# Kernel tuning notes

Hardware: AMD Instinct MI355X
Metric: run time of the kernel (lower is better)

The kernel has to match this reference:

```python
import jax, jax.numpy as jnp
import numpy as np
import math

NFREQ = 257
NFILTERS = 64
IN_DIM = 64
HIDDEN = 128
SR = 16000
B = 2
T = 1000


def _mel_bounds():
    # Exact replica of FreqCompression.__init__ bound computation (htk mel scale).
    all_freqs = np.linspace(0.0, SR // 2, NFREQ)
    m_max = 2595.0 * math.log10(1.0 + (SR / 2.0) / 700.0)
    m_pts = np.linspace(0.0, m_max, NFILTERS + 2)
    f_pts = 700.0 * (10.0 ** (m_pts / 2595.0) - 1.0)
    bounds = [0]
    for i in range(1, NFILTERS + 1):
        bounds.append(int(np.argmax(all_freqs > f_pts[i])))
    bounds.append(NFREQ)
    return bounds


def setup_inputs() -> dict:
    key = jax.random.key(0)
    k1, k2 = jax.random.split(key)
    bounds = _mel_bounds()
    widths = np.array([bounds[f + 2] - bounds[f] for f in range(NFILTERS)])
    jmax = int(widths.max())
    starts = np.array(bounds[:NFILTERS])
    # per-band freq-bin gather indices, clamped padding
    idx = np.clip(starts[:, None] + np.arange(jmax)[None, :], 0, NFREQ - 1)
    mask = (np.arange(jmax)[None, :] < widths[:, None]).astype(np.float32)  # (F, Jmax)
    x = jax.random.normal(k1, (B, IN_DIM, T, NFREQ), dtype=jnp.float32)
    # Padded ragged trans1 weights: band f uses a (HIDDEN, width_f*IN_DIM) Linear (no bias).
    # Zero-masked beyond each band's true width so padded gather lanes contribute nothing.
    W = jax.random.normal(k2, (NFILTERS, HIDDEN, IN_DIM, jmax), dtype=jnp.float32) * 0.05
    W = W * jnp.asarray(mask)[:, None, None, :]
    return {"x": x, "W": W, "idx": jnp.asarray(idx, jnp.int32), "inverse": 0}


def reference(x, W, idx, inverse):
    # Forward (compression) branch of FreqCompression.forward (inverse == 0).
    # Original: x -> (B, T, in_dim, F); per band f: flatten x[..., bounds[f]:bounds[f+2]]
    # over (in_dim, width) and apply bias-free Linear -> (B, T, hidden); stack over bands
    # and permute to (B, hidden, T, nfilters). Expressed as one padded gather + einsum:
    # x: (B, C, T, F_full); idx: (F, J); W: (F, H, C, J) zero-masked past band width.
    xg = x[:, :, :, idx]  # (B, C, T, F, J)
    out = jnp.einsum('bctfj,fhcj->bhtf', xg, W)  # (B, H, T, F)
    return out
```

## Files before the change

### kernel.cpp

```cpp
#include <hip/hip_runtime.h>
#include <hip/hip_bf16.h>

#define B_    2
#define C_    64
#define T_    1000
#define NF_   257
#define F_    64
#define H_    128
#define NFP_  288

typedef __bf16  bfv8  __attribute__((ext_vector_type(8)));
typedef float   f32x4 __attribute__((ext_vector_type(4)));
typedef short   s16x8 __attribute__((ext_vector_type(8)));

#define GLOBAL_AS __attribute__((address_space(1)))
#define SHARED_AS __attribute__((address_space(3)))

static __device__ __forceinline__ short f2bf(float f) {
  __hip_bfloat16 h = __float2bfloat16(f);
  return *reinterpret_cast<short*>(&h);
}

static __device__ __forceinline__ void gload_lds16(const void* g, void* l) {
  __builtin_amdgcn_global_load_lds((const GLOBAL_AS void*)g, (SHARED_AS void*)l, 16, 0, 0);
}

__global__ __launch_bounds__(256) void xprep_kernel(const float* __restrict__ x,
                                                    short* __restrict__ xT) {
  __shared__ float Ls[64][33];
  const int k0 = blockIdx.x * 32;
  const int t  = blockIdx.y;
  const int b  = blockIdx.z;
  {
    const int k  = threadIdx.x & 31;
    const int cb = threadIdx.x >> 5;
#pragma unroll
    for (int i = 0; i < 8; ++i) {
      int c = cb + 8 * i;
      float f = 0.0f;
      int kk = k0 + k;
      if (kk < NF_) f = x[(((size_t)(b * C_ + c)) * T_ + t) * NF_ + kk];
      Ls[c][k] = f;
    }
  }
  __syncthreads();
  {
    const int k  = threadIdx.x >> 3;
    const int c0 = (threadIdx.x & 7) * 8;
    s16x8 v;
#pragma unroll
    for (int i = 0; i < 8; ++i) v[i] = f2bf(Ls[c0 + i][k]);
    *reinterpret_cast<s16x8*>(&xT[(((size_t)(b * T_ + t)) * NFP_ + k0 + k) * C_ + c0]) = v;
  }
}

__global__ __launch_bounds__(256) void wprep_kernel(const float* __restrict__ W,
                                                    short* __restrict__ Wp,
                                                    int* __restrict__ wwidth,
                                                    int jmax, int JPAD) {
  extern __shared__ short Lw[];
  __shared__ int smax;
  const int f  = blockIdx.x >> 4;
  const int h8 = (blockIdx.x & 15) * 8;
  const int tid = threadIdx.x;
  if (tid == 0) smax = 0;
  __syncthreads();
  const int chunk = 8 * C_ * jmax;
  const float* src = W + ((size_t)(f * H_ + h8)) * C_ * jmax;
  int lm = -1;
  for (int o = tid; o < chunk; o += 256) {
    float v = src[o];
    Lw[o] = f2bf(v);
    if (v != 0.0f) { int j = o % jmax; if (j > lm) lm = j; }
  }
  atomicMax(&smax, lm + 1);
  __syncthreads();
  if (tid == 0) atomicMax(&wwidth[f], smax);
  const int KP = C_ * JPAD;
  const int nv = 8 * JPAD * 8;
  for (int id = tid; id < nv; id += 256) {
    int c0 = (id & 7) * 8;
    int j  = (id >> 3) % JPAD;
    int h  = (id >> 3) / JPAD;
    s16x8 v;
    if (j < jmax) {
#pragma unroll
      for (int u = 0; u < 8; ++u) v[u] = Lw[h * C_ * jmax + (c0 + u) * jmax + j];
    } else {
      short z = f2bf(0.0f);
#pragma unroll
      for (int u = 0; u < 8; ++u) v[u] = z;
    }
    *reinterpret_cast<s16x8*>(&Wp[((size_t)(f * H_ + h8 + h)) * KP + j * C_ + c0]) = v;
  }
}

__global__ __launch_bounds__(256) void gemm_kernel(const short* __restrict__ xT,
                                                   const short* __restrict__ Wp,
                                                   const int* __restrict__ idx,
                                                   const int* __restrict__ wwidth,
                                                   float* __restrict__ tmp,
                                                   int jmax, int JPAD) {
  __shared__ short As[128 * 64];
  __shared__ short Ws[128 * 64];
  const int id = blockIdx.x;
  const int sw = (id & 7) * 128 + (id >> 3);
  const int f  = sw & 63;
  const int tb = sw >> 6;
  const int tt = tb & 7;
  const int b  = tb >> 3;
  const int t0 = tt * 128;
  const int tid  = threadIdx.x;
  const int wave = tid >> 6;
  const int lane = tid & 63;
  const int wm = wave >> 1, wn = wave & 1;
  const int start = idx[f * jmax];
  const int KP = C_ * JPAD;
  int wf = wwidth[f];
  if (wf > JPAD) wf = JPAD;

  f32x4 acc[4][4] = {};

  const int srow = wave * 32 + (lane >> 3);
  const int scol = (lane & 7) * 8;

  for (int j = 0; j < wf; ++j) {
    __syncthreads();
#pragma unroll
    for (int i = 0; i < 4; ++i) {
      int r = srow + i * 8;
      int tc = t0 + r; if (tc >= T_) tc = T_ - 1;
      const short* src = &xT[(((size_t)(b * T_ + tc)) * NFP_ + (start + j)) * C_ + scol];
      gload_lds16(src, &As[(wave * 32 + i * 8) * 64]);
    }
#pragma unroll
    for (int i = 0; i < 4; ++i) {
      int h = srow + i * 8;
      const short* src = &Wp[((size_t)(f * H_ + h)) * KP + j * 64 + scol];
      gload_lds16(src, &Ws[(wave * 32 + i * 8) * 64]);
    }
    __syncthreads();
#pragma unroll
    for (int ks = 0; ks < 2; ++ks) {
      bfv8 a[4], w[4];
#pragma unroll
      for (int mi = 0; mi < 4; ++mi)
        a[mi] = *reinterpret_cast<const bfv8*>(
            &As[(wm * 64 + mi * 16 + (lane & 15)) * 64 + ks * 32 + (lane >> 4) * 8]);
#pragma unroll
      for (int ni = 0; ni < 4; ++ni)
        w[ni] = *reinterpret_cast<const bfv8*>(
            &Ws[(wn * 64 + ni * 16 + (lane & 15)) * 64 + ks * 32 + (lane >> 4) * 8]);
#pragma unroll
      for (int mi = 0; mi < 4; ++mi)
#pragma unroll
        for (int ni = 0; ni < 4; ++ni)
          acc[mi][ni] = __builtin_amdgcn_mfma_f32_16x16x32_bf16(a[mi], w[ni], acc[mi][ni], 0, 0, 0);
    }
  }

  float* obase = tmp + ((size_t)(b * F_ + f)) * T_ * H_;
#pragma unroll
  for (int mi = 0; mi < 4; ++mi) {
#pragma unroll
    for (int q = 0; q < 4; ++q) {
      int t = t0 + wm * 64 + mi * 16 + (lane >> 4) * 4 + q;
      if (t < T_) {
#pragma unroll
        for (int ni = 0; ni < 4; ++ni) {
          int h = wn * 64 + ni * 16 + (lane & 15);
          obase[(size_t)t * H_ + h] = acc[mi][ni][q];
        }
      }
    }
  }
}

__global__ __launch_bounds__(256) void trans_kernel(const float* __restrict__ tmp,
                                                    float* __restrict__ out) {
  __shared__ float L[64][129];
  const int t = blockIdx.x;
  const int b = blockIdx.y;
  {
    const int h  = threadIdx.x & 127;
    const int f0 = threadIdx.x >> 7;
#pragma unroll
    for (int i = 0; i < 32; ++i) {
      int fo = f0 * 32 + i;
      L[fo][h] = tmp[(((size_t)(b * F_ + fo)) * T_ + t) * H_ + h];
    }
  }
  __syncthreads();
  {
    const int fo = threadIdx.x & 63;
    const int h0 = threadIdx.x >> 6;
#pragma unroll
    for (int i = 0; i < 32; ++i) {
      int h = h0 * 32 + i;
      out[(((size_t)(b * H_ + h)) * T_ + t) * F_ + fo] = L[fo][h];
    }
  }
}

__global__ __launch_bounds__(256) void naive_kernel(const float* __restrict__ x,
                                                    const float* __restrict__ W,
                                                    const int* __restrict__ idx,
                                                    float* __restrict__ out,
                                                    int jmax, size_t n) {
  size_t o = (size_t)blockIdx.x * 256 + threadIdx.x;
  if (o >= n) return;
  int f = (int)(o & 63);
  size_t r = o >> 6;
  int t = (int)(r % T_); r /= T_;
  int h = (int)(r % H_);
  int b = (int)(r / H_);
  float s = 0.0f;
  for (int c = 0; c < C_; ++c) {
    const float* xr = x + (((size_t)(b * C_ + c)) * T_ + t) * NF_;
    const float* wr = W + (((size_t)(f * H_ + h)) * C_ + c) * jmax;
    for (int j = 0; j < jmax; ++j) s += xr[idx[f * jmax + j]] * wr[j];
  }
  out[o] = s;
}

extern "C" void kernel_launch(void* const* d_in, const int* in_sizes, int n_in,
                              void* d_out, int out_size, void* d_ws, size_t ws_size,
                              hipStream_t stream) {
  const float* x  = (const float*)d_in[0];
  const float* W  = (const float*)d_in[1];
  const int* idx  = (const int*)d_in[2];
  float* out      = (float*)d_out;

  const int jmax = in_sizes[2] / F_;
  const int JPAD = (jmax + 7) & ~7;

  const size_t xbytes = (size_t)B_ * T_ * NFP_ * C_ * 2;
  const size_t wbytes = (size_t)F_ * H_ * C_ * JPAD * 2;
  const size_t tbytes = (size_t)B_ * F_ * T_ * H_ * 4;
  const size_t wwbytes = 256;
  const size_t lws = (size_t)8 * C_ * jmax * 2;

  if (JPAD <= 32 && ws_size >= xbytes + wbytes + tbytes + wwbytes && lws <= 48 * 1024) {
    short* xT   = (short*)d_ws;
    short* Wp   = (short*)((char*)d_ws + xbytes);
    float* tmp  = (float*)((char*)d_ws + xbytes + wbytes);
    int* wwidth = (int*)((char*)d_ws + xbytes + wbytes + tbytes);

    hipLaunchKernelGGL(xprep_kernel, dim3(NFP_ / 32, T_, B_), dim3(256), 0, stream, x, xT);
    hipLaunchKernelGGL(wprep_kernel, dim3(F_ * 16), dim3(256), lws, stream,
                       W, Wp, wwidth, jmax, JPAD);
    hipLaunchKernelGGL(gemm_kernel, dim3(1024), dim3(256), 0, stream,
                       xT, Wp, idx, wwidth, tmp, jmax, JPAD);
    hipLaunchKernelGGL(trans_kernel, dim3(T_, B_), dim3(256), 0, stream, tmp, out);
  } else {
    const size_t n = (size_t)B_ * H_ * T_ * F_;
    hipLaunchKernelGGL(naive_kernel, dim3((unsigned)((n + 255) / 256)), dim3(256), 0, stream,
                       x, W, idx, out, jmax, n);
  }
}
```

Baseline: 352.5 us.

## Double-buffer GEMM LDS staging with swizzle and store bf16 intermediate

The GEMM kernel now double-buffers the A and W tiles in LDS. It prefetches two K-steps ahead with global_load_lds and uses manual vmcnt waits and s_barrier, so loads overlap the MFMA work. An XOR swizzle on LDS columns is meant to remove bank conflicts on the fragment reads. The intermediate tmp buffer is also stored as bf16 instead of fp32, which halves the traffic between the GEMM and transpose kernels but adds another rounding step to the output.

```diff
diff --git a/kernel.cpp b/kernel.cpp
--- a/kernel.cpp
+++ b/kernel.cpp
@@ -19,6 +19,10 @@
 static __device__ __forceinline__ short f2bf(float f) {
   __hip_bfloat16 h = __float2bfloat16(f);
   return *reinterpret_cast<short*>(&h);
+}
+static __device__ __forceinline__ float bf2f(short s) {
+  __hip_bfloat16 h = *reinterpret_cast<__hip_bfloat16*>(&s);
+  return __bfloat162float(h);
 }
 
 static __device__ __forceinline__ void gload_lds16(const void* g, void* l) {
@@ -99,10 +103,10 @@
                                                    const short* __restrict__ Wp,
                                                    const int* __restrict__ idx,
                                                    const int* __restrict__ wwidth,
-                                                   float* __restrict__ tmp,
+                                                   short* __restrict__ tmp,
                                                    int jmax, int JPAD) {
-  __shared__ short As[128 * 64];
-  __shared__ short Ws[128 * 64];
+  __shared__ short As[2][128 * 64];
+  __shared__ short Ws[2][128 * 64];
   const int id = blockIdx.x;
   const int sw = (id & 7) * 128 + (id >> 3);
   const int f  = sw & 63;
@@ -119,47 +123,72 @@
   int wf = wwidth[f];
   if (wf > JPAD) wf = JPAD;
 
+  const int lrow = lane >> 3;
+  const int lsw  = ((lane & 7) ^ lrow) * 8;
+  const int l7   = lane & 7;
+
   f32x4 acc[4][4] = {};
 
-  const int srow = wave * 32 + (lane >> 3);
-  const int scol = (lane & 7) * 8;
+#define STAGE(J, BSEL)                                                              \
+  {                                                                                 \
+    _Pragma("unroll")                                                               \
+    for (int i = 0; i < 4; ++i) {                                                   \
+      int tc = t0 + wave * 32 + i * 8 + lrow; if (tc >= T_) tc = T_ - 1;            \
+      gload_lds16(&xT[(((size_t)(b * T_ + tc)) * NFP_ + (start + (J))) * C_ + lsw], \
+                  &As[BSEL][(wave * 32 + i * 8) * 64]);                             \
+    }                                                                               \
+    _Pragma("unroll")                                                               \
+    for (int i = 0; i < 4; ++i) {                                                   \
+      int h = wave * 32 + i * 8 + lrow;                                             \
+      gload_lds16(&Wp[((size_t)(f * H_ + h)) * KP + (J) * 64 + lsw],                \
+                  &Ws[BSEL][(wave * 32 + i * 8) * 64]);                             \
+    }                                                                               \
+  }
+
+  if (wf > 0) STAGE(0, 0);
+  if (wf > 1) STAGE(1, 1);
+  asm volatile("" ::: "memory");
+  __builtin_amdgcn_sched_barrier(0);
 
   for (int j = 0; j < wf; ++j) {
-    __syncthreads();
-#pragma unroll
-    for (int i = 0; i < 4; ++i) {
-      int r = srow + i * 8;
-      int tc = t0 + r; if (tc >= T_) tc = T_ - 1;
-      const short* src = &xT[(((size_t)(b * T_ + tc)) * NFP_ + (start + j)) * C_ + scol];
-      gload_lds16(src, &As[(wave * 32 + i * 8) * 64]);
-    }
-#pragma unroll
-    for (int i = 0; i < 4; ++i) {
-      int h = srow + i * 8;
-      const short* src = &Wp[((size_t)(f * H_ + h)) * KP + j * 64 + scol];
-      gload_lds16(src, &Ws[(wave * 32 + i * 8) * 64]);
-    }
-    __syncthreads();
+    const int cur = j & 1;
+    if (j + 1 < wf) asm volatile("s_waitcnt vmcnt(8)" ::: "memory");
+    else            asm volatile("s_waitcnt vmcnt(0)" ::: "memory");
+    __builtin_amdgcn_sched_barrier(0);
+    asm volatile("s_barrier" ::: "memory");
+    __builtin_amdgcn_sched_barrier(0);
+
 #pragma unroll
     for (int ks = 0; ks < 2; ++ks) {
       bfv8 a[4], w[4];
 #pragma unroll
-      for (int mi = 0; mi < 4; ++mi)
-        a[mi] = *reinterpret_cast<const bfv8*>(
-            &As[(wm * 64 + mi * 16 + (lane & 15)) * 64 + ks * 32 + (lane >> 4) * 8]);
-#pragma unroll
-      for (int ni = 0; ni < 4; ++ni)
-        w[ni] = *reinterpret_cast<const bfv8*>(
-            &Ws[(wn * 64 + ni * 16 + (lane & 15)) * 64 + ks * 32 + (lane >> 4) * 8]);
+      for (int mi = 0; mi < 4; ++mi) {
+        int rA = wm * 64 + mi * 16 + (lane & 15);
+        int sA = ((ks * 4 + (lane >> 4)) ^ l7) * 8;
+        a[mi] = *reinterpret_cast<const bfv8*>(&As[cur][rA * 64 + sA]);
+      }
+#pragma unroll
+      for (int ni = 0; ni < 4; ++ni) {
+        int rB = wn * 64 + ni * 16 + (lane & 15);
+        int sB = ((ks * 4 + (lane >> 4)) ^ l7) * 8;
+        w[ni] = *reinterpret_cast<const bfv8*>(&Ws[cur][rB * 64 + sB]);
+      }
 #pragma unroll
       for (int mi = 0; mi < 4; ++mi)
 #pragma unroll
         for (int ni = 0; ni < 4; ++ni)
           acc[mi][ni] = __builtin_amdgcn_mfma_f32_16x16x32_bf16(a[mi], w[ni], acc[mi][ni], 0, 0, 0);
     }
-  }
-
-  float* obase = tmp + ((size_t)(b * F_ + f)) * T_ * H_;
+
+    __builtin_amdgcn_sched_barrier(0);
+    asm volatile("s_barrier" ::: "memory");
+    __builtin_amdgcn_sched_barrier(0);
+    if (j + 2 < wf) STAGE(j + 2, cur);
+    asm volatile("" ::: "memory");
+  }
+#undef STAGE
+
+  short* obase = tmp + ((size_t)(b * F_ + f)) * T_ * H_;
 #pragma unroll
   for (int mi = 0; mi < 4; ++mi) {
 #pragma unroll
@@ -169,25 +198,28 @@
 #pragma unroll
         for (int ni = 0; ni < 4; ++ni) {
           int h = wn * 64 + ni * 16 + (lane & 15);
-          obase[(size_t)t * H_ + h] = acc[mi][ni][q];
+          obase[(size_t)t * H_ + h] = f2bf(acc[mi][ni][q]);
         }
       }
     }
   }
 }
 
-__global__ __launch_bounds__(256) void trans_kernel(const float* __restrict__ tmp,
+__global__ __launch_bounds__(256) void trans_kernel(const short* __restrict__ tmp,
                                                     float* __restrict__ out) {
   __shared__ float L[64][129];
   const int t = blockIdx.x;
   const int b = blockIdx.y;
   {
-    const int h  = threadIdx.x & 127;
-    const int f0 = threadIdx.x >> 7;
-#pragma unroll
-    for (int i = 0; i < 32; ++i) {
-      int fo = f0 * 32 + i;
-      L[fo][h] = tmp[(((size_t)(b * F_ + fo)) * T_ + t) * H_ + h];
+    const int h0 = (threadIdx.x & 15) * 8;
+    const int fb = threadIdx.x >> 4;
+#pragma unroll
+    for (int i = 0; i < 4; ++i) {
+      int f = fb + 16 * i;
+      s16x8 v = *reinterpret_cast<const s16x8*>(
+          &tmp[(((size_t)(b * F_ + f)) * T_ + t) * H_ + h0]);
+#pragma unroll
+      for (int u = 0; u < 8; ++u) L[f][h0 + u] = bf2f(v[u]);
     }
   }
   __syncthreads();
@@ -236,14 +268,14 @@
 
   const size_t xbytes = (size_t)B_ * T_ * NFP_ * C_ * 2;
   const size_t wbytes = (size_t)F_ * H_ * C_ * JPAD * 2;
-  const size_t tbytes = (size_t)B_ * F_ * T_ * H_ * 4;
+  const size_t tbytes = (size_t)B_ * F_ * T_ * H_ * 2;
   const size_t wwbytes = 256;
   const size_t lws = (size_t)8 * C_ * jmax * 2;
 
   if (JPAD <= 32 && ws_size >= xbytes + wbytes + tbytes + wwbytes && lws <= 48 * 1024) {
     short* xT   = (short*)d_ws;
     short* Wp   = (short*)((char*)d_ws + xbytes);
-    float* tmp  = (float*)((char*)d_ws + xbytes + wbytes);
+    short* tmp  = (short*)((char*)d_ws + xbytes + wbytes);
     int* wwidth = (int*)((char*)d_ws + xbytes + wbytes + tbytes);
 
     hipLaunchKernelGGL(xprep_kernel, dim3(NFP_ / 32, T_, B_), dim3(256), 0, stream, x, xT);
```

Result: faster. 339.5 us (-3.7%).
